# Kernel tuning notes

Hardware: AMD Instinct MI355X
Metric: run time of the kernel (lower is better)

The kernel has to match this reference:

```python
import jax, jax.numpy as jnp
import numpy as np

B, L, DIM, ET, NH, SD, NC = 32, 200, 36, 128, 64, 9, 2


def setup_inputs() -> dict:
    key = jax.random.key(0)
    ks = jax.random.split(key, 16)
    f = jnp.float32
    vals = jax.random.normal(ks[0], (B, L, DIM), f)
    obs = (jax.random.uniform(ks[1], (B, L, DIM)) < 0.7).astype(f)  # 0/1 observation mask
    x = jnp.concatenate([vals, obs], -1)                            # (B, L, 2*DIM)
    time_steps = jnp.sort(jax.random.uniform(ks[2], (B, L)), axis=1)
    static_info = jax.random.normal(ks[3], (B, SD), f)
    query_param = jnp.linspace(0.0, 1.0, ET, dtype=f)               # nn.Parameter(linspace)

    def lin(k, o, i, s):
        return jax.random.normal(k, (o, i), f) * s

    return dict(
        x=x, time_steps=time_steps, static_info=static_info, query_param=query_param,
        periodic_w=lin(ks[4], ET - 1, 1, 1.0), periodic_b=jnp.zeros((ET - 1,), f),
        timelin_w=lin(ks[5], 1, 1, 1.0), timelin_b=jnp.zeros((1,), f),
        qw=lin(ks[6], ET, ET, ET ** -0.5), qb=jnp.zeros((ET,), f),
        kw=lin(ks[7], ET, ET, ET ** -0.5), kb=jnp.zeros((ET,), f),
        ow=lin(ks[8], DIM, 2 * DIM, (2 * DIM) ** -0.5), ob=jnp.zeros((DIM,), f),
        gru_w_ih=lin(ks[9], 3 * NH, DIM, DIM ** -0.5),
        gru_w_hh=lin(ks[10], 3 * NH, NH, NH ** -0.5),
        gru_b_ih=jnp.zeros((3 * NH,), f), gru_b_hh=jnp.zeros((3 * NH,), f),
        st_w=lin(ks[11], 8, SD, SD ** -0.5), st_b=jnp.zeros((8,), f),
        c1_w=lin(ks[12], NH + 8, NH + 8, (NH + 8) ** -0.5), c1_b=jnp.zeros((NH + 8,), f),
        bn_g=jnp.ones((NH + 8,), f), bn_b=jnp.zeros((NH + 8,), f),
        c2_w=lin(ks[13], NC, NH + 8, (NH + 8) ** -0.5), c2_b=jnp.zeros((NC,), f),
        rand_mask=jax.random.randint(ks[14], (B, L), 0, 2, jnp.int32),
    )


def reference(x, time_steps, static_info, query_param, periodic_w, periodic_b,
              timelin_w, timelin_b, qw, qb, kw, kb, ow, ob,
              gru_w_ih, gru_w_hh, gru_b_ih, gru_b_hh, st_w, st_b,
              c1_w, c1_b, bn_g, bn_b, c2_w, c2_b, rand_mask):
    dim = x.shape[-1] // 2
    irr = x[:, :, dim:]                                   # observation mask channels
    temp = rand_mask.astype(x.dtype)[:, :, None]          # random_masking keep-mask
    m_small = irr * temp
    irr2 = jnp.concatenate([irr, irr], -1)                # (B, L, 2*dim)
    m2 = jnp.concatenate([m_small, m_small], -1)

    def time_emb(tt):
        tt = tt[..., None]
        return jnp.concatenate([tt @ timelin_w.T + timelin_b,
                                jnp.sin(tt @ periodic_w.T + periodic_b)], -1)

    key_e = time_emb(time_steps)                          # (B, L, ET)
    query_e = time_emb(query_param[None, :])[0]           # (ET, ET)
    q = query_e @ qw.T + qb                               # num_heads=1 => dk=ET
    k = key_e @ kw.T + kb
    scores = jnp.einsum('qd,bld->bql', q, k) / jnp.sqrt(jnp.asarray(ET, x.dtype))

    def mta(mask):
        # per-channel masked softmax over keys l: (B, Lq, L, 2*dim)
        s5 = jnp.where(mask[:, None, :, :] == 0, jnp.asarray(-1e9, x.dtype),
                       scores[:, :, :, None])
        p = jax.nn.softmax(s5, axis=2)
        o = jnp.einsum('bqld,bld->bqd', p, x)             # (B, Lq, 2*dim)
        return o @ ow.T + ob                              # (B, Lq, dim)

    out_te = mta(irr2)
    out1_te = mta(m2)

    sx = x[:, :, :dim]
    sx_g = jnp.round(jax.nn.sigmoid(jnp.einsum('bld,ble->bde', sx, sx)))
    sout = jax.nn.sigmoid(jnp.einsum('bqd,bqe->bde', out_te, out_te))

    def step(h, xt):  # torch GRU cell, gate order r,z,n
        gi = xt @ gru_w_ih.T + gru_b_ih
        gh = h @ gru_w_hh.T + gru_b_hh
        ir, iz, inn = jnp.split(gi, 3, -1)
        hr, hz, hn = jnp.split(gh, 3, -1)
        r = jax.nn.sigmoid(ir + hr)
        z = jax.nn.sigmoid(iz + hz)
        n = jnp.tanh(inn + r * hn)
        return (1 - z) * n + z * h, None

    h0 = jnp.zeros((x.shape[0], gru_w_hh.shape[1]), x.dtype)
    h_fin, _ = jax.lax.scan(step, h0, jnp.swapaxes(out_te, 0, 1))

    st = static_info @ st_w.T + st_b
    cls_in = jnp.concatenate([h_fin, st], 1)
    z1 = cls_in @ c1_w.T + c1_b
    mu = z1.mean(0)
    var = z1.var(0)                                       # BatchNorm1d (training stats)
    zn = (z1 - mu) / jnp.sqrt(var + 1e-5) * bn_g + bn_b
    zg = jax.nn.gelu(zn, approximate=False)
    logits = zg @ c2_w.T + c2_b
    return (out_te, out1_te, logits, sx_g, sout, query_param)
```

## Files before the change

### kernel.cpp

```cpp
#include <hip/hip_runtime.h>

#define B_   32
#define L_   200
#define DIM_ 36
#define ET_  128
#define NH_  64
#define SD_  9
#define NC_  2

#define O_TE   0
#define O_T1   147456
#define O_LG   294912
#define O_SXG  294976
#define O_SOUT 336448
#define O_QP   377920

typedef __fp16 half_t;
typedef __attribute__((ext_vector_type(2))) __fp16 half2_t;

__device__ __forceinline__ float sigm(float x) { return 1.f / (1.f + expf(-x)); }
__device__ __forceinline__ float fsigm(float x) {
  return __builtin_amdgcn_rcpf(1.f + __expf(-x));
}
__device__ __forceinline__ float ftanh(float x) {
  return 2.f * __builtin_amdgcn_rcpf(1.f + __expf(-2.f * x)) - 1.f;
}
__device__ __forceinline__ half2_t f2h2(float a, float b) {
  return __builtin_amdgcn_cvt_pkrtz(a, b);
}
__device__ __forceinline__ float dot2acc(half2_t w, half2_t h, float acc) {
#if __has_builtin(__builtin_amdgcn_fdot2)
  return __builtin_amdgcn_fdot2(w, h, acc, false);
#else
  return acc + (float)w.x * (float)h.x + (float)w.y * (float)h.y;
#endif
}

__global__ __launch_bounds__(256) void k_pre2(
    const float* __restrict__ qw, const float* __restrict__ kw,
    const float* __restrict__ qb, const float* __restrict__ qp,
    const float* __restrict__ pw, const float* __restrict__ pb,
    const float* __restrict__ tlw, const float* __restrict__ tlb,
    const float* __restrict__ x, float* __restrict__ qm2,
    float* __restrict__ xmean, float* __restrict__ out) {
  int blk = blockIdx.x, t = threadIdx.x;
  if (blk < 128) {
    __shared__ float eq[128];
    __shared__ float uq[128];
    int q = blk;
    if (t < 128) {
      float tt = qp[q];
      eq[t] = (t == 0) ? tt * tlw[0] + tlb[0]
                       : __sinf(tt * pw[t - 1] + pb[t - 1]);
    }
    __syncthreads();
    if (t < 128) {
      const float4* qw4 = (const float4*)(qw + (size_t)t * 128);
      float a = qb[t];
      #pragma unroll 8
      for (int c = 0; c < 32; c++) {
        float4 w = qw4[c];
        a += eq[4 * c] * w.x + eq[4 * c + 1] * w.y +
             eq[4 * c + 2] * w.z + eq[4 * c + 3] * w.w;
      }
      uq[t] = a;
    }
    __syncthreads();
    if (t < 128) {
      float a = 0.f;
      #pragma unroll 8
      for (int i = 0; i < 128; i++) a += uq[i] * kw[i * 128 + t];
      qm2[q * 128 + t] = a * 0.088388347648318447f;
      if (q == 0) out[O_QP + t] = qp[t];
    }
    return;
  }
  int b = blk - 128;
  if (t < 72) {
    float s = 0.f;
    const float* xb = x + (size_t)b * L_ * 72 + t;
    #pragma unroll 8
    for (int l = 0; l < L_; l++) s += xb[(size_t)l * 72];
    xmean[b * 72 + t] = s * (1.0f / L_);
  }
}

__global__ __launch_bounds__(1024, 1) void k_attn(
    const float* __restrict__ qm, const float* __restrict__ ts,
    const float* __restrict__ pw, const float* __restrict__ pb,
    const float* __restrict__ tlw, const float* __restrict__ tlb,
    const float* __restrict__ x, const int* __restrict__ rm,
    const float* __restrict__ xmean, const float* __restrict__ ow,
    const float* __restrict__ ob, float* __restrict__ out) {
  __shared__ __align__(16) char Abuf[103936];
  __shared__ __align__(16) float qs[16][128];
  __shared__ __align__(16) float sc[16][200];
  __shared__ __align__(16) float owsh[DIM_][72];
  float*   ksA  = (float*)Abuf;
  half2_t* wsh2 = (half2_t*)Abuf;
  float*   sums = (float*)(Abuf + 57600);
  float*   ofr  = (float*)(Abuf + 57600 + 36864);

  int b = blockIdx.x >> 3;
  int q0 = (blockIdx.x & 7) << 4;
  int tid = threadIdx.x;

  const float4* qsrc = (const float4*)(qm + q0 * ET_);
  for (int i = tid; i < 16 * 32; i += 1024) ((float4*)qs)[i] = qsrc[i];
  const float4* owsrc = (const float4*)ow;
  for (int i = tid; i < DIM_ * 18; i += 1024) ((float4*)owsh)[i] = owsrc[i];
  {
    float tl_w = tlw[0], tl_b = tlb[0];
    const float* tsb = ts + b * L_;
    for (int i = tid; i < L_ * 128; i += 1024) {
      int l = i >> 7, j = i & 127;
      float t = tsb[l];
      float e = (j == 0) ? t * tl_w + tl_b : __sinf(t * pw[j - 1] + pb[j - 1]);
      int blkj = (j >> 2) ^ ((l >> 2) & 7);
      ksA[(l << 7) + (blkj << 2) + (j & 3)] = e;
    }
  }
  __syncthreads();

  {
    int w = tid >> 6, lg = tid & 63;
    int qp2 = w >> 1;
    int lh = w & 1;
    float acc[2][2];
    #pragma unroll
    for (int i = 0; i < 2; i++)
      #pragma unroll
      for (int j = 0; j < 2; j++) acc[i][j] = 0.f;
    const float4* ks4 = (const float4*)ksA;
    const float4* qs4 = (const float4*)qs;
    int lbase = 100 * lh + 2 * lg;
    int swz0 = (lbase >> 2) & 7;
    int swz1 = ((lbase + 1) >> 2) & 7;
    #pragma unroll 4
    for (int d4 = 0; d4 < 32; d4++) {
      float4 kv[2];
      {
        int l0c = (lbase < 100 * lh + 100) ? lbase : (100 * lh + 99);
        int l1c = (lbase + 1 < 100 * lh + 100) ? lbase + 1 : (100 * lh + 99);
        kv[0] = ks4[(l0c << 5) + (d4 ^ swz0)];
        kv[1] = ks4[(l1c << 5) + (d4 ^ swz1)];
      }
      #pragma unroll
      for (int i = 0; i < 2; i++) {
        float4 qv = qs4[(2 * qp2 + i) * 32 + d4];
        #pragma unroll
        for (int j = 0; j < 2; j++)
          acc[i][j] += qv.x * kv[j].x + qv.y * kv[j].y +
                       qv.z * kv[j].z + qv.w * kv[j].w;
      }
    }
    if (2 * lg < 100) {
      #pragma unroll
      for (int i = 0; i < 2; i++) {
        float2 v = {acc[i][0], acc[i][1]};
        *((float2*)(&sc[2 * qp2 + i][lbase])) = v;
      }
    }
  }
  __syncthreads();

  {
    int qi = tid >> 6, li = tid & 63;
    float m = -1e30f;
    for (int l = li; l < L_; l += 64) m = fmaxf(m, sc[qi][l]);
    #pragma unroll
    for (int off = 32; off >= 1; off >>= 1) m = fmaxf(m, __shfl_xor(m, off));
    for (int l = li; l < L_; l += 64) sc[qi][l] = __expf(sc[qi][l] - m);
  }

  {
    const float2* xb2 = (const float2*)(x + (size_t)b * L_ * 72);
    const int* rmb = rm + b * L_;
    for (int i = tid; i < L_ * 72; i += 1024) {
      int l = i / 72, c2 = i % 72;
      int seg = c2 / 18, fh = c2 % 18;
      float2 v = xb2[l * 36 + fh];
      float2 o = xb2[l * 36 + 18 + fh];
      float rr = (float)rmb[l];
      float w0, w1;
      if (seg == 0)      { w0 = o.x * v.x;      w1 = o.y * v.y; }
      else if (seg == 1) { w0 = o.x;            w1 = o.y; }
      else if (seg == 2) { w0 = o.x * v.x * rr; w1 = o.y * v.y * rr; }
      else               { w0 = o.x * rr;       w1 = o.y * rr; }
      wsh2[l * 72 + c2] = f2h2(w0, w1);
    }
  }
  __syncthreads();

  {
    int quarter = tid >> 8, tt = tid & 255;
    int qi = tt >> 4, li = tt & 15;
    int l0 = quarter * 50;
    float accA[8], accB[8];
    #pragma unroll
    for (int k = 0; k < 8; k++) { accA[k] = 0.f; accB[k] = 0.f; }
    const float4* wA = (const float4*)wsh2;
    #pragma unroll 2
    for (int l = l0; l < l0 + 50; l++) {
      float ev = sc[qi][l];
      float4 wa = wA[l * 18 + li];
      union { float f; half2_t h; } u0, u1, u2, u3;
      u0.f = wa.x; u1.f = wa.y; u2.f = wa.z; u3.f = wa.w;
      accA[0] += ev * (float)u0.h.x; accA[1] += ev * (float)u0.h.y;
      accA[2] += ev * (float)u1.h.x; accA[3] += ev * (float)u1.h.y;
      accA[4] += ev * (float)u2.h.x; accA[5] += ev * (float)u2.h.y;
      accA[6] += ev * (float)u3.h.x; accA[7] += ev * (float)u3.h.y;
      if (li < 2) {
        float4 wb = wA[l * 18 + 16 + li];
        union { float f; half2_t h; } b0, b1, b2, b3;
        b0.f = wb.x; b1.f = wb.y; b2.f = wb.z; b3.f = wb.w;
        accB[0] += ev * (float)b0.h.x; accB[1] += ev * (float)b0.h.y;
        accB[2] += ev * (float)b1.h.x; accB[3] += ev * (float)b1.h.y;
        accB[4] += ev * (float)b2.h.x; accB[5] += ev * (float)b2.h.y;
        accB[6] += ev * (float)b3.h.x; accB[7] += ev * (float)b3.h.y;
      }
    }
    float* sq = sums + quarter * 2304 + qi * 144;
    float4* sA = (float4*)(sq + 8 * li);
    sA[0] = make_float4(accA[0], accA[1], accA[2], accA[3]);
    sA[1] = make_float4(accA[4], accA[5], accA[6], accA[7]);
    if (li < 2) {
      float4* sB = (float4*)(sq + 128 + 8 * li);
      sB[0] = make_float4(accB[0], accB[1], accB[2], accB[3]);
      sB[1] = make_float4(accB[4], accB[5], accB[6], accB[7]);
    }
  }
  __syncthreads();

  const float* xm = xmean + b * 72;
  for (int idx = tid; idx < 16 * DIM_; idx += 1024) {
    int qq = idx / DIM_, j = idx % DIM_;
    const float* s0 = sums + qq * 144;
    const float* s1 = s0 + 2304;
    const float* s2 = s1 + 2304;
    const float* s3 = s2 + 2304;
    float numA = (s0[j] + s1[j]) + (s2[j] + s3[j]);
    float denA = (s0[36 + j] + s1[36 + j]) + (s2[36 + j] + s3[36 + j]);
    float numB = (s0[72 + j] + s1[72 + j]) + (s2[72 + j] + s3[72 + j]);
    float denB = (s0[108 + j] + s1[108 + j]) + (s2[108 + j] + s3[108 + j]);
    float al, ah, bl, bh;
    if (denA > 0.f) { al = numA / denA; ah = 1.f; }
    else            { al = xm[j];       ah = xm[36 + j]; }
    if (denB > 0.f) { bl = numB / denB; bh = 1.f; }
    else            { bl = xm[j];       bh = xm[36 + j]; }
    float* oq = ofr + qq * 144;
    oq[j] = al;      oq[36 + j] = ah;
    oq[72 + j] = bl; oq[108 + j] = bh;
  }
  __syncthreads();

  for (int idx = tid; idx < 16 * 72; idx += 1024) {
    int qq = idx / 72, t = idx % 72;
    int v = t / DIM_, i2 = t % DIM_;
    const float4* o4 = (const float4*)(ofr + qq * 144 + v * 72);
    const float4* w4 = (const float4*)(owsh[i2]);
    float a = ob[i2];
    #pragma unroll
    for (int d4 = 0; d4 < 18; d4++) {
      float4 ov = o4[d4], wv = w4[d4];
      a += ov.x * wv.x + ov.y * wv.y + ov.z * wv.z + ov.w * wv.w;
    }
    size_t off = ((size_t)b * ET_ + q0 + qq) * DIM_ + i2;
    out[(v == 0 ? O_TE : O_T1) + off] = a;
  }
}

__global__ __launch_bounds__(256, 1) void k_sg(
    const float* __restrict__ out_ro, const float* __restrict__ x,
    const float* __restrict__ wih, const float* __restrict__ bih,
    const float* __restrict__ whh, const float* __restrict__ bhh,
    const float* __restrict__ si, const float* __restrict__ stw,
    const float* __restrict__ stb, const float* __restrict__ c1w,
    const float* __restrict__ c1b, const float* __restrict__ bng,
    const float* __restrict__ bnb, const float* __restrict__ c2w,
    const float* __restrict__ c2b,
    float* __restrict__ hfin, int* __restrict__ ctr,
    float* __restrict__ out) {
  __shared__ __align__(16) float ote_s[ET_][DIM_];
  __shared__ float gis[ET_][3 * NH_];
  __shared__ __align__(16) half2_t hpk[NH_ / 2];
  int blk = blockIdx.x, t = threadIdx.x;

  if (blk >= 64) {
    float* base = &gis[0][0];
    float (*cin)[72] = (float(*)[72])(base);
    float (*z1)[72]  = (float(*)[72])(base + 2304);
    float (*zg)[72]  = (float(*)[72])(base + 4608);
    float* c1wt = base + 6912;
    float* c2ws = base + 6912 + 5184;
    float* bngs = c2ws + 144;
    float* bnbs = bngs + 72;
    for (int idx = t; idx < 72 * 72; idx += 256) {
      int j = idx / 72, d = idx % 72;
      c1wt[d * 72 + j] = c1w[idx];
    }
    for (int idx = t; idx < NC_ * 72; idx += 256) c2ws[idx] = c2w[idx];
    if (t < 72) { bngs[t] = bng[t]; bnbs[t] = bnb[t]; }
    for (int idx = t; idx < B_ * 8; idx += 256) {
      int b = idx / 8, j = idx % 8;
      float acc = stb[j];
      #pragma unroll
      for (int d = 0; d < SD_; d++) acc += si[b * SD_ + d] * stw[j * SD_ + d];
      cin[b][NH_ + j] = acc;
    }
    __syncthreads();
    if (t == 0) {
      while (__hip_atomic_load(ctr, __ATOMIC_ACQUIRE,
                               __HIP_MEMORY_SCOPE_AGENT) < 32)
        __builtin_amdgcn_s_sleep(8);
    }
    __syncthreads();
    for (int idx = t; idx < B_ * NH_; idx += 256)
      cin[idx / NH_][idx % NH_] = hfin[idx];
    __syncthreads();
    for (int idx = t; idx < B_ * 72; idx += 256) {
      int b = idx / 72, j = idx % 72;
      float acc = c1b[j];
      #pragma unroll 8
      for (int d = 0; d < 72; d++) acc += cin[b][d] * c1wt[d * 72 + j];
      z1[b][j] = acc;
    }
    __syncthreads();
    if (t < 72) {
      float mu = 0.f;
      for (int b = 0; b < B_; b++) mu += z1[b][t];
      mu *= (1.f / B_);
      float vv = 0.f;
      for (int b = 0; b < B_; b++) { float d = z1[b][t] - mu; vv += d * d; }
      vv *= (1.f / B_);
      float inv = 1.f / sqrtf(vv + 1e-5f);
      float g = bngs[t], bb = bnbs[t];
      for (int b = 0; b < B_; b++) {
        float zn = (z1[b][t] - mu) * inv * g + bb;
        zg[b][t] = 0.5f * zn * (1.f + erff(zn * 0.70710678118654752f));
      }
    }
    __syncthreads();
    for (int idx = t; idx < B_ * NC_; idx += 256) {
      int b = idx / NC_, c = idx % NC_;
      float acc = c2b[c];
      #pragma unroll 8
      for (int d = 0; d < 72; d++) acc += zg[b][d] * c2ws[c * 72 + d];
      out[O_LG + idx] = acc;
    }
    return;
  }

  if (blk < 32) {
    int b = blk;
    float* sxs = (float*)gis;
    const float4* osrc = (const float4*)(out_ro + O_TE + (size_t)b * ET_ * DIM_);
    for (int idx = t; idx < ET_ * 9; idx += 256)
      ((float4*)&ote_s[0][0])[idx] = osrc[idx];
    const float4* xsrc = (const float4*)(x + (size_t)b * L_ * 72);
    for (int idx = t; idx < L_ * 18; idx += 256) {
      int l = idx / 18, c = idx % 18;
      ((float4*)&sxs[l * 76])[c] = xsrc[idx];
    }
    __syncthreads();
    for (int idx = t; idx < DIM_ * DIM_; idx += 256) {
      int d = idx / DIM_, e = idx % DIM_;
      float s = 0.f;
      #pragma unroll 8
      for (int q = 0; q < ET_; q++) s += ote_s[q][d] * ote_s[q][e];
      out[O_SOUT + (size_t)b * DIM_ * DIM_ + idx] = sigm(s);
    }
    for (int idx = t; idx < DIM_ * DIM_; idx += 256) {
      int d = idx / DIM_, e = idx % DIM_;
      float s = 0.f;
      #pragma unroll 8
      for (int l = 0; l < L_; l++) s += sxs[l * 76 + d] * sxs[l * 76 + e];
      out[O_SXG + (size_t)b * DIM_ * DIM_ + idx] = rintf(sigm(s));
    }
    return;
  }

  int b = blk - 32;
  const float* ote = out_ro + O_TE;
  const float4* osrc = (const float4*)(ote + (size_t)b * ET_ * DIM_);
  for (int idx = t; idx < ET_ * DIM_ / 4; idx += 256)
    ((float4*)&ote_s[0][0])[idx] = osrc[idx];
  __syncthreads();

  if (t < 3 * NH_) {
    float wv[DIM_];
    const float* wrow = wih + (size_t)t * DIM_;
    #pragma unroll
    for (int d = 0; d < DIM_; d++) wv[d] = wrow[d];
    float bi = bih[t] + ((t < 2 * NH_) ? bhh[t] : 0.f);
    for (int q = 0; q < ET_; q++) {
      const float4* xr = (const float4*)ote_s[q];
      float a = bi;
      #pragma unroll
      for (int c = 0; c < 9; c++) {
        float4 xv = xr[c];
        a += xv.x * wv[4 * c] + xv.y * wv[4 * c + 1] +
             xv.z * wv[4 * c + 2] + xv.w * wv[4 * c + 3];
      }
      gis[q][t] = a;
    }
  }
  __syncthreads();
  if (t >= 64) return;

  half2_t wr[32], wz[32], wn[32];
  {
    const float2* r0 = (const float2*)(whh + (size_t)t * NH_);
    const float2* r1 = (const float2*)(whh + (size_t)(NH_ + t) * NH_);
    const float2* r2 = (const float2*)(whh + (size_t)(2 * NH_ + t) * NH_);
    #pragma unroll
    for (int c = 0; c < 32; c++) {
      float2 a = r0[c], bb = r1[c], cc = r2[c];
      wr[c] = f2h2(a.x, a.y);
      wz[c] = f2h2(bb.x, bb.y);
      wn[c] = f2h2(cc.x, cc.y);
    }
  }
  float bh_n = bhh[2 * NH_ + t];

  float h = 0.f;
  ((half_t*)hpk)[t] = (half_t)0.f;
  for (int q = 0; q < ET_; q++) {
    float gi_r = gis[q][t];
    float gi_z = gis[q][NH_ + t];
    float gi_n = gis[q][2 * NH_ + t];
    float ar = 0.f, az = 0.f, an = 0.f;
    const float4* hp4 = (const float4*)hpk;
    #pragma unroll
    for (int c4 = 0; c4 < 8; c4++) {
      float4 hv = hp4[c4];
      union { float f; half2_t h; } u0, u1, u2, u3;
      u0.f = hv.x; u1.f = hv.y; u2.f = hv.z; u3.f = hv.w;
      int c = c4 * 4;
      ar = dot2acc(wr[c + 0], u0.h, ar);
      az = dot2acc(wz[c + 0], u0.h, az);
      an = dot2acc(wn[c + 0], u0.h, an);
      ar = dot2acc(wr[c + 1], u1.h, ar);
      az = dot2acc(wz[c + 1], u1.h, az);
      an = dot2acc(wn[c + 1], u1.h, an);
      ar = dot2acc(wr[c + 2], u2.h, ar);
      az = dot2acc(wz[c + 2], u2.h, az);
      an = dot2acc(wn[c + 2], u2.h, an);
      ar = dot2acc(wr[c + 3], u3.h, ar);
      az = dot2acc(wz[c + 3], u3.h, az);
      an = dot2acc(wn[c + 3], u3.h, an);
    }
    float r = fsigm(gi_r + ar);
    float z = fsigm(gi_z + az);
    float n = ftanh(gi_n + r * (an + bh_n));
    h = n + z * (h - n);
    ((half_t*)hpk)[t] = (half_t)h;
  }
  hfin[b * NH_ + t] = h;
  __threadfence();
  if (t == 0) atomicAdd(ctr, 1);
}

extern "C" void kernel_launch(void* const* d_in, const int* in_sizes, int n_in,
                              void* d_out, int out_size, void* d_ws,
                              size_t ws_size, hipStream_t stream) {
  const float* x    = (const float*)d_in[0];
  const float* ts   = (const float*)d_in[1];
  const float* si   = (const float*)d_in[2];
  const float* qp   = (const float*)d_in[3];
  const float* pw   = (const float*)d_in[4];
  const float* pb   = (const float*)d_in[5];
  const float* tlw  = (const float*)d_in[6];
  const float* tlb  = (const float*)d_in[7];
  const float* qw   = (const float*)d_in[8];
  const float* qb   = (const float*)d_in[9];
  const float* kw   = (const float*)d_in[10];
  const float* ow   = (const float*)d_in[12];
  const float* ob   = (const float*)d_in[13];
  const float* wih  = (const float*)d_in[14];
  const float* whh  = (const float*)d_in[15];
  const float* bih  = (const float*)d_in[16];
  const float* bhh  = (const float*)d_in[17];
  const float* stw  = (const float*)d_in[18];
  const float* stb  = (const float*)d_in[19];
  const float* c1w  = (const float*)d_in[20];
  const float* c1b  = (const float*)d_in[21];
  const float* bng  = (const float*)d_in[22];
  const float* bnb  = (const float*)d_in[23];
  const float* c2w  = (const float*)d_in[24];
  const float* c2b  = (const float*)d_in[25];
  const int*   rm   = (const int*)d_in[26];

  float* out = (float*)d_out;

  float* W = (float*)d_ws;
  float* ws_qm2   = W;
  float* ws_xmean = W + 16384;
  float* ws_hfin  = W + 18688;
  int*   ws_ctr   = (int*)(W + 20736);

  hipMemsetAsync(ws_ctr, 0, sizeof(int), stream);
  hipLaunchKernelGGL(k_pre2, dim3(160), dim3(256), 0, stream,
                     qw, kw, qb, qp, pw, pb, tlw, tlb, x, ws_qm2, ws_xmean,
                     out);
  hipLaunchKernelGGL(k_attn, dim3(B_ * 8), dim3(1024), 0, stream,
                     ws_qm2, ts, pw, pb, tlw, tlb, x, rm, ws_xmean, ow, ob,
                     out);
  hipLaunchKernelGGL(k_sg, dim3(65), dim3(256), 0, stream,
                     out, x, wih, bih, whh, bhh, si, stw, stb, c1w, c1b,
                     bng, bnb, c2w, c2b, ws_hfin, ws_ctr, out);
}
```

Measured before the change: 228.1 us.

## Split attention kernel into smaller blocks with chunked L processing

The attention kernel now runs 512 blocks of 512 threads, each handling 8 queries instead of 16. It processes the 200 keys in two chunks of 100, which halves shared memory so several blocks can share a CU. The aim is better occupancy and latency hiding. In exchange, each block recomputes the sinusoidal key embedding and the masked value tiles, so that redundant work doubles, and the chunked loops add extra barriers.

```diff
diff --git a/kernel.cpp b/kernel.cpp
--- a/kernel.cpp
+++ b/kernel.cpp
@@ -85,84 +85,66 @@
   }
 }
 
-__global__ __launch_bounds__(1024, 1) void k_attn(
+__global__ __launch_bounds__(512, 4) void k_attn(
     const float* __restrict__ qm, const float* __restrict__ ts,
     const float* __restrict__ pw, const float* __restrict__ pb,
     const float* __restrict__ tlw, const float* __restrict__ tlb,
     const float* __restrict__ x, const int* __restrict__ rm,
     const float* __restrict__ xmean, const float* __restrict__ ow,
     const float* __restrict__ ob, float* __restrict__ out) {
-  __shared__ __align__(16) char Abuf[103936];
-  __shared__ __align__(16) float qs[16][128];
-  __shared__ __align__(16) float sc[16][200];
-  __shared__ __align__(16) float owsh[DIM_][72];
+  __shared__ __align__(16) char Abuf[52992];
+  __shared__ __align__(16) float qs[8][128];
+  __shared__ __align__(16) float sc[8][200];
   float*   ksA  = (float*)Abuf;
   half2_t* wsh2 = (half2_t*)Abuf;
-  float*   sums = (float*)(Abuf + 57600);
-  float*   ofr  = (float*)(Abuf + 57600 + 36864);
-
-  int b = blockIdx.x >> 3;
-  int q0 = (blockIdx.x & 7) << 4;
+  float*   sums = (float*)(Abuf + 28800);
+  float*   ofr  = (float*)(Abuf + 38016);
+  float*   owsh = (float*)(Abuf + 42624);
+
+  int b  = blockIdx.x >> 4;
+  int qo = blockIdx.x & 15;
+  int q0 = qo << 3;
   int tid = threadIdx.x;
 
-  const float4* qsrc = (const float4*)(qm + q0 * ET_);
-  for (int i = tid; i < 16 * 32; i += 1024) ((float4*)qs)[i] = qsrc[i];
-  const float4* owsrc = (const float4*)ow;
-  for (int i = tid; i < DIM_ * 18; i += 1024) ((float4*)owsh)[i] = owsrc[i];
+  float tl_w = tlw[0], tl_b = tlb[0];
+  const float* tsb = ts + b * L_;
+
   {
-    float tl_w = tlw[0], tl_b = tlb[0];
-    const float* tsb = ts + b * L_;
-    for (int i = tid; i < L_ * 128; i += 1024) {
+    const float4* qsrc = (const float4*)(qm + q0 * ET_);
+    for (int i = tid; i < 8 * 32; i += 512) ((float4*)qs)[i] = qsrc[i];
+  }
+  for (int ck = 0; ck < 2; ck++) {
+    for (int i = tid; i < 100 * 128; i += 512) {
       int l = i >> 7, j = i & 127;
-      float t = tsb[l];
+      float t = tsb[ck * 100 + l];
       float e = (j == 0) ? t * tl_w + tl_b : __sinf(t * pw[j - 1] + pb[j - 1]);
       int blkj = (j >> 2) ^ ((l >> 2) & 7);
       ksA[(l << 7) + (blkj << 2) + (j & 3)] = e;
     }
-  }
-  __syncthreads();
-
-  {
-    int w = tid >> 6, lg = tid & 63;
-    int qp2 = w >> 1;
-    int lh = w & 1;
-    float acc[2][2];
-    #pragma unroll
-    for (int i = 0; i < 2; i++)
-      #pragma unroll
-      for (int j = 0; j < 2; j++) acc[i][j] = 0.f;
-    const float4* ks4 = (const float4*)ksA;
-    const float4* qs4 = (const float4*)qs;
-    int lbase = 100 * lh + 2 * lg;
-    int swz0 = (lbase >> 2) & 7;
-    int swz1 = ((lbase + 1) >> 2) & 7;
-    #pragma unroll 4
-    for (int d4 = 0; d4 < 32; d4++) {
-      float4 kv[2];
-      {
-        int l0c = (lbase < 100 * lh + 100) ? lbase : (100 * lh + 99);
-        int l1c = (lbase + 1 < 100 * lh + 100) ? lbase + 1 : (100 * lh + 99);
-        kv[0] = ks4[(l0c << 5) + (d4 ^ swz0)];
-        kv[1] = ks4[(l1c << 5) + (d4 ^ swz1)];
+    __syncthreads();
+    {
+      int w = tid >> 6, lg = tid & 63;
+      int qp2 = w >> 1, lh = w & 1;
+      if (lg < 50) {
+        int lloc = 50 * lh + lg;
+        int swz = (lloc >> 2) & 7;
+        float acc0 = 0.f, acc1 = 0.f;
+        const float4* ks4 = (const float4*)ksA;
+        const float4* qs4 = (const float4*)qs;
+        #pragma unroll 4
+        for (int d4 = 0; d4 < 32; d4++) {
+          float4 kv = ks4[(lloc << 5) + (d4 ^ swz)];
+          float4 qv0 = qs4[(2 * qp2 + 0) * 32 + d4];
+          float4 qv1 = qs4[(2 * qp2 + 1) * 32 + d4];
+          acc0 += qv0.x * kv.x + qv0.y * kv.y + qv0.z * kv.z + qv0.w * kv.w;
+          acc1 += qv1.x * kv.x + qv1.y * kv.y + qv1.z * kv.z + qv1.w * kv.w;
+        }
+        sc[2 * qp2 + 0][ck * 100 + lloc] = acc0;
+        sc[2 * qp2 + 1][ck * 100 + lloc] = acc1;
       }
-      #pragma unroll
-      for (int i = 0; i < 2; i++) {
-        float4 qv = qs4[(2 * qp2 + i) * 32 + d4];
-        #pragma unroll
-        for (int j = 0; j < 2; j++)
-          acc[i][j] += qv.x * kv[j].x + qv.y * kv[j].y +
-                       qv.z * kv[j].z + qv.w * kv[j].w;
-      }
-    }
-    if (2 * lg < 100) {
-      #pragma unroll
-      for (int i = 0; i < 2; i++) {
-        float2 v = {acc[i][0], acc[i][1]};
-        *((float2*)(&sc[2 * qp2 + i][lbase])) = v;
-      }
-    }
-  }
-  __syncthreads();
+    }
+    __syncthreads();
+  }
 
   {
     int qi = tid >> 6, li = tid & 63;
@@ -172,16 +154,24 @@
     for (int off = 32; off >= 1; off >>= 1) m = fmaxf(m, __shfl_xor(m, off));
     for (int l = li; l < L_; l += 64) sc[qi][l] = __expf(sc[qi][l] - m);
   }
-
-  {
-    const float2* xb2 = (const float2*)(x + (size_t)b * L_ * 72);
-    const int* rmb = rm + b * L_;
-    for (int i = tid; i < L_ * 72; i += 1024) {
+  __syncthreads();
+
+  const float2* xb2 = (const float2*)(x + (size_t)b * L_ * 72);
+  const int* rmb = rm + b * L_;
+  int sub = tid >> 8, tt = tid & 255;
+  int qi = tt >> 5, li = tt & 31;
+  float accW[8];
+  #pragma unroll
+  for (int k = 0; k < 8; k++) accW[k] = 0.f;
+
+  for (int ck = 0; ck < 2; ck++) {
+    for (int i = tid; i < 100 * 72; i += 512) {
       int l = i / 72, c2 = i % 72;
+      int lg_ = ck * 100 + l;
       int seg = c2 / 18, fh = c2 % 18;
-      float2 v = xb2[l * 36 + fh];
-      float2 o = xb2[l * 36 + 18 + fh];
-      float rr = (float)rmb[l];
+      float2 v = xb2[lg_ * 36 + fh];
+      float2 o = xb2[lg_ * 36 + 18 + fh];
+      float rr = (float)rmb[lg_];
       float w0, w1;
       if (seg == 0)      { w0 = o.x * v.x;      w1 = o.y * v.y; }
       else if (seg == 1) { w0 = o.x;            w1 = o.y; }
@@ -189,60 +179,44 @@
       else               { w0 = o.x * rr;       w1 = o.y * rr; }
       wsh2[l * 72 + c2] = f2h2(w0, w1);
     }
+    if (ck == 0) {
+      const float4* owsrc = (const float4*)ow;
+      for (int i = tid; i < DIM_ * 18; i += 512) ((float4*)owsh)[i] = owsrc[i];
+    }
+    __syncthreads();
+    if (li < 18) {
+      const float4* wA = (const float4*)wsh2;
+      #pragma unroll 2
+      for (int l = 0; l < 50; l++) {
+        int lW = sub * 50 + l;
+        float ev = sc[qi][ck * 100 + lW];
+        float4 wa = wA[lW * 18 + li];
+        union { float f; half2_t h; } u0, u1, u2, u3;
+        u0.f = wa.x; u1.f = wa.y; u2.f = wa.z; u3.f = wa.w;
+        accW[0] += ev * (float)u0.h.x; accW[1] += ev * (float)u0.h.y;
+        accW[2] += ev * (float)u1.h.x; accW[3] += ev * (float)u1.h.y;
+        accW[4] += ev * (float)u2.h.x; accW[5] += ev * (float)u2.h.y;
+        accW[6] += ev * (float)u3.h.x; accW[7] += ev * (float)u3.h.y;
+      }
+    }
+    __syncthreads();
+  }
+  if (li < 18) {
+    float* sq = sums + sub * 1152 + qi * 144 + 8 * li;
+    ((float4*)sq)[0] = make_float4(accW[0], accW[1], accW[2], accW[3]);
+    ((float4*)sq)[1] = make_float4(accW[4], accW[5], accW[6], accW[7]);
   }
   __syncthreads();
 
-  {
-    int quarter = tid >> 8, tt = tid & 255;
-    int qi = tt >> 4, li = tt & 15;
-    int l0 = quarter * 50;
-    float accA[8], accB[8];
-    #pragma unroll
-    for (int k = 0; k < 8; k++) { accA[k] = 0.f; accB[k] = 0.f; }
-    const float4* wA = (const float4*)wsh2;
-    #pragma unroll 2
-    for (int l = l0; l < l0 + 50; l++) {
-      float ev = sc[qi][l];
-      float4 wa = wA[l * 18 + li];
-      union { float f; half2_t h; } u0, u1, u2, u3;
-      u0.f = wa.x; u1.f = wa.y; u2.f = wa.z; u3.f = wa.w;
-      accA[0] += ev * (float)u0.h.x; accA[1] += ev * (float)u0.h.y;
-      accA[2] += ev * (float)u1.h.x; accA[3] += ev * (float)u1.h.y;
-      accA[4] += ev * (float)u2.h.x; accA[5] += ev * (float)u2.h.y;
-      accA[6] += ev * (float)u3.h.x; accA[7] += ev * (float)u3.h.y;
-      if (li < 2) {
-        float4 wb = wA[l * 18 + 16 + li];
-        union { float f; half2_t h; } b0, b1, b2, b3;
-        b0.f = wb.x; b1.f = wb.y; b2.f = wb.z; b3.f = wb.w;
-        accB[0] += ev * (float)b0.h.x; accB[1] += ev * (float)b0.h.y;
-        accB[2] += ev * (float)b1.h.x; accB[3] += ev * (float)b1.h.y;
-        accB[4] += ev * (float)b2.h.x; accB[5] += ev * (float)b2.h.y;
-        accB[6] += ev * (float)b3.h.x; accB[7] += ev * (float)b3.h.y;
-      }
-    }
-    float* sq = sums + quarter * 2304 + qi * 144;
-    float4* sA = (float4*)(sq + 8 * li);
-    sA[0] = make_float4(accA[0], accA[1], accA[2], accA[3]);
-    sA[1] = make_float4(accA[4], accA[5], accA[6], accA[7]);
-    if (li < 2) {
-      float4* sB = (float4*)(sq + 128 + 8 * li);
-      sB[0] = make_float4(accB[0], accB[1], accB[2], accB[3]);
-      sB[1] = make_float4(accB[4], accB[5], accB[6], accB[7]);
-    }
-  }
-  __syncthreads();
-
   const float* xm = xmean + b * 72;
-  for (int idx = tid; idx < 16 * DIM_; idx += 1024) {
+  for (int idx = tid; idx < 8 * DIM_; idx += 512) {
     int qq = idx / DIM_, j = idx % DIM_;
     const float* s0 = sums + qq * 144;
-    const float* s1 = s0 + 2304;
-    const float* s2 = s1 + 2304;
-    const float* s3 = s2 + 2304;
-    float numA = (s0[j] + s1[j]) + (s2[j] + s3[j]);
-    float denA = (s0[36 + j] + s1[36 + j]) + (s2[36 + j] + s3[36 + j]);
-    float numB = (s0[72 + j] + s1[72 + j]) + (s2[72 + j] + s3[72 + j]);
-    float denB = (s0[108 + j] + s1[108 + j]) + (s2[108 + j] + s3[108 + j]);
+    const float* s1 = s0 + 1152;
+    float numA = s0[j] + s1[j];
+    float denA = s0[36 + j] + s1[36 + j];
+    float numB = s0[72 + j] + s1[72 + j];
+    float denB = s0[108 + j] + s1[108 + j];
     float al, ah, bl, bh;
     if (denA > 0.f) { al = numA / denA; ah = 1.f; }
     else            { al = xm[j];       ah = xm[36 + j]; }
@@ -254,11 +228,11 @@
   }
   __syncthreads();
 
-  for (int idx = tid; idx < 16 * 72; idx += 1024) {
+  for (int idx = tid; idx < 8 * 72; idx += 512) {
     int qq = idx / 72, t = idx % 72;
     int v = t / DIM_, i2 = t % DIM_;
     const float4* o4 = (const float4*)(ofr + qq * 144 + v * 72);
-    const float4* w4 = (const float4*)(owsh[i2]);
+    const float4* w4 = (const float4*)(owsh + i2 * 72);
     float a = ob[i2];
     #pragma unroll
     for (int d4 = 0; d4 < 18; d4++) {
@@ -503,7 +477,7 @@
   hipLaunchKernelGGL(k_pre2, dim3(160), dim3(256), 0, stream,
                      qw, kw, qb, qp, pw, pb, tlw, tlb, x, ws_qm2, ws_xmean,
                      out);
-  hipLaunchKernelGGL(k_attn, dim3(B_ * 8), dim3(1024), 0, stream,
+  hipLaunchKernelGGL(k_attn, dim3(B_ * 16), dim3(512), 0, stream,
                      ws_qm2, ts, pw, pb, tlw, tlb, x, rm, ws_xmean, ow, ob,
                      out);
   hipLaunchKernelGGL(k_sg, dim3(65), dim3(256), 0, stream,
```

After: 235.9 us. +3.4%, slower.

## Precompute per-batch key embeddings and value weights once in prologue kernel

Applied to the files above, without the earlier changes.

The sinusoidal key-time embedding and the masked half-precision value matrix were each recomputed by all 8 query-block CTAs of the same batch inside the attention kernel. They are now computed once per batch by extra blocks of the prologue kernel and stored in workspace in the already-swizzled layout, and the attention kernel only copies them into shared memory with float4 loads. This removes redundant sin and elementwise work from the attention kernel, at the cost of extra global-memory traffic (about 4 MB written and then read back) and a larger prologue grid.

```diff
diff --git a/kernel.cpp b/kernel.cpp
--- a/kernel.cpp
+++ b/kernel.cpp
@@ -41,8 +41,11 @@
     const float* __restrict__ qb, const float* __restrict__ qp,
     const float* __restrict__ pw, const float* __restrict__ pb,
     const float* __restrict__ tlw, const float* __restrict__ tlb,
-    const float* __restrict__ x, float* __restrict__ qm2,
-    float* __restrict__ xmean, float* __restrict__ out) {
+    const float* __restrict__ ts, const float* __restrict__ x,
+    const int* __restrict__ rm,
+    float* __restrict__ qm2, float* __restrict__ xmean,
+    float* __restrict__ ks_ws, half2_t* __restrict__ w_ws,
+    float* __restrict__ out) {
   int blk = blockIdx.x, t = threadIdx.x;
   if (blk < 128) {
     __shared__ float eq[128];
@@ -75,21 +78,56 @@
     }
     return;
   }
-  int b = blk - 128;
-  if (t < 72) {
-    float s = 0.f;
-    const float* xb = x + (size_t)b * L_ * 72 + t;
-    #pragma unroll 8
-    for (int l = 0; l < L_; l++) s += xb[(size_t)l * 72];
-    xmean[b * 72 + t] = s * (1.0f / L_);
+  if (blk < 160) {
+    int b = blk - 128;
+    if (t < 72) {
+      float s = 0.f;
+      const float* xb = x + (size_t)b * L_ * 72 + t;
+      #pragma unroll 8
+      for (int l = 0; l < L_; l++) s += xb[(size_t)l * 72];
+      xmean[b * 72 + t] = s * (1.0f / L_);
+    }
+    return;
+  }
+  if (blk < 224) {
+    int bb = (blk - 160) >> 1, half = (blk - 160) & 1;
+    float tl_w = tlw[0], tl_b = tlb[0];
+    const float* tsb = ts + bb * L_;
+    float* dst = ks_ws + (size_t)bb * 25600;
+    for (int i = half * 12800 + t; i < half * 12800 + 12800; i += 256) {
+      int l = i >> 7, j = i & 127;
+      float tt = tsb[l];
+      float e = (j == 0) ? tt * tl_w + tl_b
+                         : __sinf(tt * pw[j - 1] + pb[j - 1]);
+      int blkj = (j >> 2) ^ ((l >> 2) & 7);
+      dst[(l << 7) + (blkj << 2) + (j & 3)] = e;
+    }
+    return;
+  }
+  {
+    int bb = blk - 224;
+    const float2* xb2 = (const float2*)(x + (size_t)bb * L_ * 72);
+    const int* rmb = rm + bb * L_;
+    half2_t* wd = w_ws + (size_t)bb * 14400;
+    for (int i = t; i < L_ * 72; i += 256) {
+      int l = i / 72, c2 = i % 72;
+      int seg = c2 / 18, fh = c2 % 18;
+      float2 v = xb2[l * 36 + fh];
+      float2 o = xb2[l * 36 + 18 + fh];
+      float rr = (float)rmb[l];
+      float w0, w1;
+      if (seg == 0)      { w0 = o.x * v.x;      w1 = o.y * v.y; }
+      else if (seg == 1) { w0 = o.x;            w1 = o.y; }
+      else if (seg == 2) { w0 = o.x * v.x * rr; w1 = o.y * v.y * rr; }
+      else               { w0 = o.x * rr;       w1 = o.y * rr; }
+      wd[l * 72 + c2] = f2h2(w0, w1);
+    }
   }
 }
 
 __global__ __launch_bounds__(1024, 1) void k_attn(
-    const float* __restrict__ qm, const float* __restrict__ ts,
-    const float* __restrict__ pw, const float* __restrict__ pb,
-    const float* __restrict__ tlw, const float* __restrict__ tlb,
-    const float* __restrict__ x, const int* __restrict__ rm,
+    const float* __restrict__ qm, const float* __restrict__ ks_ws,
+    const half2_t* __restrict__ w_ws,
     const float* __restrict__ xmean, const float* __restrict__ ow,
     const float* __restrict__ ob, float* __restrict__ out) {
   __shared__ __align__(16) char Abuf[103936];
@@ -110,15 +148,8 @@
   const float4* owsrc = (const float4*)ow;
   for (int i = tid; i < DIM_ * 18; i += 1024) ((float4*)owsh)[i] = owsrc[i];
   {
-    float tl_w = tlw[0], tl_b = tlb[0];
-    const float* tsb = ts + b * L_;
-    for (int i = tid; i < L_ * 128; i += 1024) {
-      int l = i >> 7, j = i & 127;
-      float t = tsb[l];
-      float e = (j == 0) ? t * tl_w + tl_b : __sinf(t * pw[j - 1] + pb[j - 1]);
-      int blkj = (j >> 2) ^ ((l >> 2) & 7);
-      ksA[(l << 7) + (blkj << 2) + (j & 3)] = e;
-    }
+    const float4* kssrc = (const float4*)(ks_ws + (size_t)b * 25600);
+    for (int i = tid; i < 6400; i += 1024) ((float4*)ksA)[i] = kssrc[i];
   }
   __syncthreads();
 
@@ -174,21 +205,8 @@
   }
 
   {
-    const float2* xb2 = (const float2*)(x + (size_t)b * L_ * 72);
-    const int* rmb = rm + b * L_;
-    for (int i = tid; i < L_ * 72; i += 1024) {
-      int l = i / 72, c2 = i % 72;
-      int seg = c2 / 18, fh = c2 % 18;
-      float2 v = xb2[l * 36 + fh];
-      float2 o = xb2[l * 36 + 18 + fh];
-      float rr = (float)rmb[l];
-      float w0, w1;
-      if (seg == 0)      { w0 = o.x * v.x;      w1 = o.y * v.y; }
-      else if (seg == 1) { w0 = o.x;            w1 = o.y; }
-      else if (seg == 2) { w0 = o.x * v.x * rr; w1 = o.y * v.y * rr; }
-      else               { w0 = o.x * rr;       w1 = o.y * rr; }
-      wsh2[l * 72 + c2] = f2h2(w0, w1);
-    }
+    const float4* wsrc = (const float4*)(w_ws + (size_t)b * 14400);
+    for (int i = tid; i < 3600; i += 1024) ((float4*)wsh2)[i] = wsrc[i];
   }
   __syncthreads();
 
@@ -494,18 +512,19 @@
   float* out = (float*)d_out;
 
   float* W = (float*)d_ws;
-  float* ws_qm2   = W;
-  float* ws_xmean = W + 16384;
-  float* ws_hfin  = W + 18688;
-  int*   ws_ctr   = (int*)(W + 20736);
+  float*   ws_qm2   = W;
+  float*   ws_xmean = W + 16384;
+  float*   ws_hfin  = W + 18688;
+  int*     ws_ctr   = (int*)(W + 20736);
+  float*   ws_ks    = W + 20800;
+  half2_t* ws_w     = (half2_t*)(W + 20800 + 819200);
 
   hipMemsetAsync(ws_ctr, 0, sizeof(int), stream);
-  hipLaunchKernelGGL(k_pre2, dim3(160), dim3(256), 0, stream,
-                     qw, kw, qb, qp, pw, pb, tlw, tlb, x, ws_qm2, ws_xmean,
-                     out);
+  hipLaunchKernelGGL(k_pre2, dim3(256), dim3(256), 0, stream,
+                     qw, kw, qb, qp, pw, pb, tlw, tlb, ts, x, rm,
+                     ws_qm2, ws_xmean, ws_ks, ws_w, out);
   hipLaunchKernelGGL(k_attn, dim3(B_ * 8), dim3(1024), 0, stream,
-                     ws_qm2, ts, pw, pb, tlw, tlb, x, rm, ws_xmean, ow, ob,
-                     out);
+                     ws_qm2, ws_ks, ws_w, ws_xmean, ow, ob, out);
   hipLaunchKernelGGL(k_sg, dim3(65), dim3(256), 0, stream,
                      out, x, wih, bih, whh, bhh, si, stw, stb, c1w, c1b,
                      bng, bnb, c2w, c2b, ws_hfin, ws_ctr, out);
```

Result: no change. 226.4 us (-0.8%).
